# Performance work log

Measured on AMD Instinct MI355X. Metric: run time of the kernel, lower is better.

Reference implementation:

```python
import jax, jax.numpy as jnp
import numpy as np

BINS = 10


def _neg_pearson(p, t):
    # global standardization (torch.std default is unbiased, ddof=1)
    p = (p - p.mean()) / p.std(ddof=1)
    t = (t - t.mean()) / t.std(ddof=1)
    N = p.shape[1]
    sx = p.sum(1); sy = t.sum(1)
    sxy = (p * t).sum(1)
    sx2 = (p * p).sum(1); sy2 = (t * t).sum(1)
    pear = (N * sxy - sx * sy) / jnp.sqrt((N * sx2 - sx**2) * (N * sy2 - sy**2))
    return (1.0 - pear).mean()


def _hann(N):
    # torch.hann_window is periodic: 0.5*(1 - cos(2*pi*n/N))
    return 0.5 * (1.0 - jnp.cos(2.0 * jnp.pi * jnp.arange(N, dtype=jnp.float32) / N))


def _phase_correlation(x, t):
    # torch.stft with n_fft=seq_len, center=False, hann window -> single frame = rfft(x*hann)
    N = x.shape[1]
    w = _hann(N)
    xf = jnp.fft.rfft(x * w, axis=1)   # [B, N//2+1]
    tf = jnp.fft.rfft(t * w, axis=1)
    corr = xf * jnp.conj(tf)
    corr = corr / jnp.abs(corr)        # phase-only correlation
    cm = jnp.fft.irfft(corr, n=N, axis=1)  # [B, N]
    idx = jnp.argmax(cm, axis=1)
    return 1.0 - jnp.mean(jnp.cos(2.0 * jnp.pi * idx / N))


def _power_spectrum(x, t):
    xp = jnp.abs(jnp.fft.rfft(x, axis=1)) ** 2
    tp = jnp.abs(jnp.fft.rfft(t, axis=1)) ** 2
    return jnp.mean(jnp.abs(xp - tp)) / jnp.mean(tp)


def _mutual_information(x, y, bins=BINS):
    B, S = x.shape
    xmin = x.min(1); xmax = x.max(1)
    ymin = y.min(1); ymax = y.max(1)
    bwx = (xmax - xmin) / bins
    bwy = (ymax - ymin) / bins
    ix = jnp.clip(((x - xmin[:, None]) / bwx[:, None]).astype(jnp.int32), 0, bins - 1)
    iy = jnp.clip(((y - ymin[:, None]) / bwy[:, None]).astype(jnp.int32), 0, bins - 1)
    flat = ix * bins + iy  # [B, S]
    # vectorized 2D histogram via scatter-add (replaces the python double loop)
    hist = jax.vmap(lambda f: jnp.zeros(bins * bins, jnp.float32).at[f].add(1.0))(flat)
    hist = hist.reshape(B, bins, bins)
    hx = hist.sum(2); hy = hist.sum(1)
    denom = B * S  # NOTE: original normalizes by batch*seq (faithful reproduction)
    px = hx / denom; py = hy / denom; pxy = hist / denom
    eps = 1e-8
    mi = (pxy * jnp.log((pxy + eps) / (px[:, :, None] * py[:, None, :] + eps))).sum((1, 2))
    hxe = -(px * jnp.log(px + eps)).sum(1)
    hye = -(py * jnp.log(py + eps)).sum(1)
    nmi = mi / ((hxe + hye) / 2.0)
    return 1.0 - nmi.mean()


def setup_inputs() -> dict:
    key = jax.random.key(0)
    k1, k2 = jax.random.split(key)
    return {
        "predictions": jax.random.normal(k1, (2, 512, 16384), dtype=jnp.float32),
        "targets": jax.random.normal(k2, (512, 16384), dtype=jnp.float32),
        "i": 0,
        "epoch": 700,
    }


def reference(predictions, targets, i, epoch):
    p = predictions[i]  # [B, S]
    loss = _neg_pearson(p, targets)
    if epoch >= 400:
        loss = loss + _phase_correlation(p, targets)
        loss = loss + _power_spectrum(p, targets)
    if epoch >= 700:
        loss = loss + _mutual_information(p, targets)
    return loss
```

## Files before the change

kernel.cpp:

```cpp
#include <hip/hip_runtime.h>
#include <math.h>

#define BB 512
#define SS 16384
#define TPIF 6.28318530717958647692f

#define PD(i) ((i) + ((i) >> 4) + ((i) >> 8))
#define NPD 17472

__device__ __forceinline__ int digrev4(int n) {
    unsigned x = __brev((unsigned)n) >> (32 - 14);
    return (int)(((x & 0x1555u) << 1) | ((x >> 1) & 0x1555u));
}


template <int SGN, int LOG2Q>
__device__ __forceinline__ void stage_dif4(float2* sz, int t) {
    constexpr int Q = 1 << LOG2Q;
    const float sg = (float)SGN;
    #pragma unroll 2
    for (int c = 0; c < 4; ++c) {
        const int j = t + (c << 10);
        const int g = j >> LOG2Q;
        const int p = j & (Q - 1);
        const int e0 = (g << (LOG2Q + 2)) + p;
        const int i0 = PD(e0);
        const int i1 = PD(e0 + Q);
        const int i2 = PD(e0 + 2 * Q);
        const int i3 = PD(e0 + 3 * Q);
        float2 z0 = sz[i0], z1 = sz[i1], z2 = sz[i2], z3 = sz[i3];
        float t0r = z0.x + z2.x, t0i = z0.y + z2.y;
        float t1r = z0.x - z2.x, t1i = z0.y - z2.y;
        float t2r = z1.x + z3.x, t2i = z1.y + z3.y;
        float t3r = z1.x - z3.x, t3i = z1.y - z3.y;
        float b0r = t0r + t2r, b0i = t0i + t2i;
        float b2r = t0r - t2r, b2i = t0i - t2i;
        float b1r = t1r - sg * t3i, b1i = t1i + sg * t3r;
        float b3r = t1r + sg * t3i, b3i = t1i - sg * t3r;
        const float a = sg * (float)p * (1.0f / (4.0f * (float)Q));
        const float cb = __builtin_amdgcn_cosf(a);
        const float sb = __builtin_amdgcn_sinf(a);
        const float w2r = cb * cb - sb * sb, w2i = 2.0f * cb * sb;
        const float w3r = cb * w2r - sb * w2i, w3i = cb * w2i + sb * w2r;
        sz[i0] = make_float2(b0r, b0i);
        sz[i1] = make_float2(b1r * cb - b1i * sb,   b1r * sb + b1i * cb);
        sz[i2] = make_float2(b2r * w2r - b2i * w2i, b2r * w2i + b2i * w2r);
        sz[i3] = make_float2(b3r * w3r - b3i * w3i, b3r * w3i + b3i * w3r);
    }
    __syncthreads();
}

template <int SGN, int LOG2Q>
__device__ __forceinline__ void stage_dit4(float2* sz, int t) {
    constexpr int Q = 1 << LOG2Q;
    const float sg = (float)SGN;
    #pragma unroll 2
    for (int c = 0; c < 4; ++c) {
        const int j = t + (c << 10);
        const int g = j >> LOG2Q;
        const int p = j & (Q - 1);
        const int e0 = (g << (LOG2Q + 2)) + p;
        const int i0 = PD(e0);
        const int i1 = PD(e0 + Q);
        const int i2 = PD(e0 + 2 * Q);
        const int i3 = PD(e0 + 3 * Q);
        float2 z0 = sz[i0], z1 = sz[i1], z2 = sz[i2], z3 = sz[i3];
        const float a = sg * (float)p * (1.0f / (4.0f * (float)Q));
        const float cb = __builtin_amdgcn_cosf(a);
        const float sb = __builtin_amdgcn_sinf(a);
        const float w2r = cb * cb - sb * sb, w2i = 2.0f * cb * sb;
        const float w3r = cb * w2r - sb * w2i, w3i = cb * w2i + sb * w2r;
        float a1r = z1.x * cb - z1.y * sb,   a1i = z1.x * sb + z1.y * cb;
        float a2r = z2.x * w2r - z2.y * w2i, a2i = z2.x * w2i + z2.y * w2r;
        float a3r = z3.x * w3r - z3.y * w3i, a3i = z3.x * w3i + z3.y * w3r;
        float t0r = z0.x + a2r, t0i = z0.y + a2i;
        float t1r = z0.x - a2r, t1i = z0.y - a2i;
        float t2r = a1r + a3r, t2i = a1i + a3i;
        float t3r = a1r - a3r, t3i = a1i - a3i;
        sz[i0] = make_float2(t0r + t2r, t0i + t2i);
        sz[i2] = make_float2(t0r - t2r, t0i - t2i);
        sz[i1] = make_float2(t1r - sg * t3i, t1i + sg * t3r);
        sz[i3] = make_float2(t1r + sg * t3i, t1i - sg * t3r);
    }
    __syncthreads();
}

__global__ __launch_bounds__(1024, 4) void k_main(const float* __restrict__ pred,
                                                  const float* __restrict__ targ,
                                                  const int* __restrict__ ip,
                                                  float* __restrict__ wpear,
                                                  float* __restrict__ wcos,
                                                  double* __restrict__ wnum,
                                                  double* __restrict__ wden,
                                                  float* __restrict__ wnmi) {
    __shared__ float2 sz[NPD];
    __shared__ double dpart[16 * 5];
    __shared__ float fpart[16 * 4];
    __shared__ int   subhist[400];
    __shared__ float hxm[10], hym[10];
    __shared__ float mterm[128];
    __shared__ float sbounds[4];
    __shared__ float svalw[16];
    __shared__ int   sidxw[16];

    const int row = blockIdx.x;
    const int t = threadIdx.x;
    const int w = t >> 6;
    const int lane = t & 63;

    const float* xg = pred + (size_t)ip[0] * (size_t)BB * SS + (size_t)row * SS;
    const float* yg = targ + (size_t)row * SS;

    {
        const float4* xg4 = reinterpret_cast<const float4*>(xg);
        const float4* yg4 = reinterpret_cast<const float4*>(yg);
        double sx = 0, sy = 0, sxy = 0, sxx = 0, syy = 0;
        float xmn = 3.4e38f, xmx = -3.4e38f, ymn = 3.4e38f, ymx = -3.4e38f;
        #pragma unroll
        for (int m2 = 0; m2 < 4; ++m2) {
            int idx = t + (m2 << 10);
            float4 a = xg4[idx];
            float4 b = yg4[idx];
            int n0 = idx << 2;
            sz[PD(n0 + 0)] = make_float2(a.x, b.x);
            sz[PD(n0 + 1)] = make_float2(a.y, b.y);
            sz[PD(n0 + 2)] = make_float2(a.z, b.z);
            sz[PD(n0 + 3)] = make_float2(a.w, b.w);
            float av[4] = {a.x, a.y, a.z, a.w};
            float bv[4] = {b.x, b.y, b.z, b.w};
            #pragma unroll
            for (int c = 0; c < 4; ++c) {
                float aa = av[c], bb = bv[c];
                sx += (double)aa; sy += (double)bb;
                sxy += (double)aa * (double)bb;
                sxx += (double)aa * (double)aa;
                syy += (double)bb * (double)bb;
                xmn = fminf(xmn, aa); xmx = fmaxf(xmx, aa);
                ymn = fminf(ymn, bb); ymx = fmaxf(ymx, bb);
            }
        }
        #pragma unroll
        for (int o = 32; o > 0; o >>= 1) {
            sx += __shfl_down(sx, o, 64);  sy += __shfl_down(sy, o, 64);
            sxy += __shfl_down(sxy, o, 64);
            sxx += __shfl_down(sxx, o, 64); syy += __shfl_down(syy, o, 64);
            xmn = fminf(xmn, __shfl_down(xmn, o, 64));
            xmx = fmaxf(xmx, __shfl_down(xmx, o, 64));
            ymn = fminf(ymn, __shfl_down(ymn, o, 64));
            ymx = fmaxf(ymx, __shfl_down(ymx, o, 64));
        }
        if (lane == 0) {
            dpart[w*5+0] = sx; dpart[w*5+1] = sy; dpart[w*5+2] = sxy;
            dpart[w*5+3] = sxx; dpart[w*5+4] = syy;
            fpart[w*4+0] = xmn; fpart[w*4+1] = xmx; fpart[w*4+2] = ymn; fpart[w*4+3] = ymx;
        }
    }
    if (t < 400) subhist[t] = 0;
    __syncthreads();
    if (t == 0) {
        double v0=0,v1=0,v2=0,v3=0,v4=0;
        float b0=fpart[0], b1=fpart[1], b2=fpart[2], b3=fpart[3];
        for (int q = 0; q < 16; ++q) {
            v0 += dpart[q*5]; v1 += dpart[q*5+1]; v2 += dpart[q*5+2];
            v3 += dpart[q*5+3]; v4 += dpart[q*5+4];
            b0 = fminf(b0, fpart[q*4]);   b1 = fmaxf(b1, fpart[q*4+1]);
            b2 = fminf(b2, fpart[q*4+2]); b3 = fmaxf(b3, fpart[q*4+3]);
        }
        double N = (double)SS;
        double num = N * v2 - v0 * v1;
        double den = sqrt((N * v3 - v0 * v0) * (N * v4 - v1 * v1));
        wpear[row] = (float)(1.0 - num / den);
        sbounds[0] = b0; sbounds[1] = b1; sbounds[2] = b2; sbounds[3] = b3;
    }
    __syncthreads();

    {
        const float x0 = sbounds[0], bwx = (sbounds[1] - x0) / 10.0f;
        const float y0 = sbounds[2], bwy = (sbounds[3] - y0) / 10.0f;
        int* hsub = subhist + ((t >> 6) & 3) * 100;
        #pragma unroll 2
        for (int m = 0; m < 16; ++m) {
            float2 v = sz[PD(t + (m << 10))];
            int ix = (int)((v.x - x0) / bwx); ix = min(max(ix, 0), 9);
            int iy = (int)((v.y - y0) / bwy); iy = min(max(iy, 0), 9);
            atomicAdd(&hsub[ix * 10 + iy], 1);
        }
    }
    __syncthreads();
    if (t < 100) subhist[t] = subhist[t] + subhist[100+t] + subhist[200+t] + subhist[300+t];
    __syncthreads();
    if (t < 10) {
        int s1 = 0, s2 = 0;
        for (int j = 0; j < 10; ++j) { s1 += subhist[t*10+j]; s2 += subhist[j*10+t]; }
        hxm[t] = (float)s1; hym[t] = (float)s2;
    }
    __syncthreads();
    {
        float term = 0.0f;
        if (t < 100) {
            const float denom = 8388608.0f, eps = 1e-8f;
            float pxy = (float)subhist[t] / denom;
            float px = hxm[t / 10] / denom, py = hym[t % 10] / denom;
            term = pxy * logf((pxy + eps) / (px * py + eps));
        }
        if (t < 128) mterm[t] = (t < 100) ? term : 0.0f;
    }
    __syncthreads();
    if (t == 0) {
        const float denom = 8388608.0f, eps = 1e-8f;
        float mi = 0.0f;
        for (int q = 0; q < 100; ++q) mi += mterm[q];
        float hxe = 0.0f, hye = 0.0f;
        for (int q = 0; q < 10; ++q) {
            float px = hxm[q] / denom, py = hym[q] / denom;
            hxe -= px * logf(px + eps);
            hye -= py * logf(py + eps);
        }
        wnmi[row] = mi / (0.5f * (hxe + hye));
    }
    __syncthreads();

    stage_dif4<-1, 12>(sz, t);
    stage_dif4<-1, 10>(sz, t);
    stage_dif4<-1,  8>(sz, t);
    stage_dif4<-1,  6>(sz, t);
    stage_dif4<-1,  4>(sz, t);
    stage_dif4<-1,  2>(sz, t);
    stage_dif4<-1,  0>(sz, t);

    {
        double anum = 0.0, aden = 0.0;
        float crv[8], civ[8];
        #pragma unroll 1
        for (int m = 0; m < 8; ++m) {
            int k = t + (m << 10);
            int km = (SS - k) & (SS - 1);
            int qa = digrev4(k), qb = digrev4(km);
            float2 za = sz[PD(qa)];
            float2 zb = sz[PD(qb)];
            float ar  = za.x, ai  = za.y;
            float cr0 = zb.x, ci0 = zb.y;
            float xr = 0.5f * (ar + cr0), xi = 0.5f * (ai - ci0);
            float yr = 0.5f * (ai + ci0), yi = 0.5f * (cr0 - ar);
            float xp = xr * xr + xi * xi;
            float tp = yr * yr + yi * yi;
            anum += (double)fabsf(xp - tp);
            aden += (double)tp;
            float2 zap = sz[PD(digrev4((k + 1) & (SS - 1)))];
            float2 zam = sz[PD(digrev4((k - 1) & (SS - 1)))];
            float2 zbp = sz[PD(digrev4((km + 1) & (SS - 1)))];
            float2 zbm = sz[PD(digrev4((km - 1) & (SS - 1)))];
            float zwr = 0.5f * ar  - 0.25f * (zap.x + zam.x);
            float zwi = 0.5f * ai  - 0.25f * (zap.y + zam.y);
            float vwr = 0.5f * cr0 - 0.25f * (zbp.x + zbm.x);
            float vwi = 0.5f * ci0 - 0.25f * (zbp.y + zbm.y);
            float xwr = 0.5f * (zwr + vwr), xwi = 0.5f * (zwi - vwi);
            float ywr = 0.5f * (zwi + vwi), ywi = 0.5f * (vwr - zwr);
            float cr = xwr * ywr + xwi * ywi;
            float ci = xwi * ywr - xwr * ywi;
            float mag = sqrtf(cr * cr + ci * ci);
            crv[m] = cr / mag; civ[m] = ci / mag;
        }
        float c8 = 0.0f;
        if (t == 0) {
            float2 z0 = sz[PD(digrev4(8192))];
            float2 zp = sz[PD(digrev4(8193))];
            float2 zm = sz[PD(digrev4(8191))];
            float ar = z0.x, ai = z0.y;
            anum += (double)fabsf(ar * ar - ai * ai);
            aden += (double)(ai * ai);
            float zwr = 0.5f * ar - 0.25f * (zp.x + zm.x);
            float zwi = 0.5f * ai - 0.25f * (zp.y + zm.y);
            float pr = zwr * zwi;
            c8 = pr / fabsf(pr);
        }
        #pragma unroll
        for (int o = 32; o > 0; o >>= 1) {
            anum += __shfl_down(anum, o, 64);
            aden += __shfl_down(aden, o, 64);
        }
        if (lane == 0) { dpart[w*2] = anum; dpart[w*2+1] = aden; }
        __syncthreads();
        #pragma unroll
        for (int m = 0; m < 8; ++m) {
            int k = t + (m << 10);
            int km = (SS - k) & (SS - 1);
            int q = digrev4(k), q2 = digrev4(km);
            sz[PD(q)]  = make_float2(crv[m],  civ[m]);
            sz[PD(q2)] = make_float2(crv[m], -civ[m]);
        }
        if (t == 0) {
            sz[PD(digrev4(8192))] = make_float2(c8, 0.0f);
            double a = 0, b = 0;
            for (int q2_ = 0; q2_ < 16; ++q2_) { a += dpart[q2_*2]; b += dpart[q2_*2+1]; }
            wnum[row] = a; wden[row] = b;
        }
    }
    __syncthreads();

    stage_dit4<1,  0>(sz, t);
    stage_dit4<1,  2>(sz, t);
    stage_dit4<1,  4>(sz, t);
    stage_dit4<1,  6>(sz, t);
    stage_dit4<1,  8>(sz, t);
    stage_dit4<1, 10>(sz, t);
    stage_dit4<1, 12>(sz, t);

    {
        float bv = -3.4e38f; int bi = 0;
        #pragma unroll
        for (int m = 0; m < 16; ++m) {
            int n = t + (m << 10);
            float v = sz[PD(n)].x;
            if (v > bv) { bv = v; bi = n; }
        }
        #pragma unroll
        for (int o = 32; o > 0; o >>= 1) {
            float v2 = __shfl_down(bv, o, 64);
            int i2 = __shfl_down(bi, o, 64);
            if (v2 > bv || (v2 == bv && i2 < bi)) { bv = v2; bi = i2; }
        }
        if (lane == 0) { svalw[w] = bv; sidxw[w] = bi; }
    }
    __syncthreads();
    if (t == 0) {
        float bv = svalw[0]; int bi = sidxw[0];
        for (int q = 1; q < 16; ++q) {
            if (svalw[q] > bv || (svalw[q] == bv && sidxw[q] < bi)) { bv = svalw[q]; bi = sidxw[q]; }
        }
        wcos[row] = cosf(TPIF * (float)bi / 16384.0f);
    }
}

__global__ __launch_bounds__(512) void k_combine(const float* __restrict__ wpear,
                                                 const float* __restrict__ wcos,
                                                 const double* __restrict__ wnum,
                                                 const double* __restrict__ wden,
                                                 const float* __restrict__ wnmi,
                                                 const int* __restrict__ ep,
                                                 float* __restrict__ out) {
    __shared__ double dp[8 * 5];
    const int tid = threadIdx.x;
    const int w = tid >> 6, lane = tid & 63;
    double v0 = (double)wpear[tid], v1 = (double)wcos[tid];
    double v2 = wnum[tid], v3 = wden[tid], v4 = (double)wnmi[tid];
    #pragma unroll
    for (int o = 32; o > 0; o >>= 1) {
        v0 += __shfl_down(v0, o, 64); v1 += __shfl_down(v1, o, 64);
        v2 += __shfl_down(v2, o, 64); v3 += __shfl_down(v3, o, 64);
        v4 += __shfl_down(v4, o, 64);
    }
    if (lane == 0) {
        dp[w*5+0] = v0; dp[w*5+1] = v1; dp[w*5+2] = v2; dp[w*5+3] = v3; dp[w*5+4] = v4;
    }
    __syncthreads();
    if (tid == 0) {
        double s0=0,s1=0,s2=0,s3=0,s4=0;
        for (int q = 0; q < 8; ++q) {
            s0 += dp[q*5]; s1 += dp[q*5+1]; s2 += dp[q*5+2]; s3 += dp[q*5+3]; s4 += dp[q*5+4];
        }
        int epoch = ep[0];
        double loss = s0 / 512.0;
        if (epoch >= 400) {
            loss += 1.0 - s1 / 512.0;
            loss += s2 / s3;
        }
        if (epoch >= 700) {
            loss += 1.0 - s4 / 512.0;
        }
        out[0] = (float)loss;
    }
}

extern "C" void kernel_launch(void* const* d_in, const int* in_sizes, int n_in,
                              void* d_out, int out_size, void* d_ws, size_t ws_size,
                              hipStream_t stream) {
    const float* pred = (const float*)d_in[0];
    const float* targ = (const float*)d_in[1];
    const int* ip = (const int*)d_in[2];
    const int* ep = (const int*)d_in[3];
    float* out = (float*)d_out;

    double* wnum = (double*)d_ws;
    double* wden = wnum + BB;
    float* wpear = (float*)(wden + BB);
    float* wcos = wpear + BB;
    float* wnmi = wcos + BB;

    k_main<<<dim3(BB), dim3(1024), 0, stream>>>(pred, targ, ip, wpear, wcos, wnum, wden, wnmi);
    k_combine<<<dim3(1), dim3(512), 0, stream>>>(wpear, wcos, wnum, wden, wnmi, ep, out);
}
```

Before: 208.3 us.

## Switch shared-memory FFT from radix-4 to radix-8 stages

Replaces the seven radix-4 DIF/DIT stages of the 16384-point in-LDS FFT with four radix-8 stages plus one twiddle-free radix-4 stage, and updates the digit-reversed index mapping to match. Fewer stages mean fewer LDS passes and fewer __syncthreads barriers. Each radix-8 butterfly also computes one sincos and derives the other twiddles by recurrence. The cost is higher register pressure per thread, under launch_bounds(1024,4), and possible bank conflicts from the new strides.

```diff
diff --git a/kernel.cpp b/kernel.cpp
--- a/kernel.cpp
+++ b/kernel.cpp
@@ -8,79 +8,171 @@
 #define PD(i) ((i) + ((i) >> 4) + ((i) >> 8))
 #define NPD 17472
 
-__device__ __forceinline__ int digrev4(int n) {
-    unsigned x = __brev((unsigned)n) >> (32 - 14);
-    return (int)(((x & 0x1555u) << 1) | ((x >> 1) & 0x1555u));
+__device__ __forceinline__ int sp(int k) {
+    int s = ((k & 7) << 11) + (((k >> 3) & 7) << 8) + (((k >> 6) & 7) << 5)
+          + (((k >> 9) & 7) << 2) + ((k >> 12) & 3);
+    return PD(s);
 }
 
 
 template <int SGN, int LOG2Q>
-__device__ __forceinline__ void stage_dif4(float2* sz, int t) {
+__device__ __forceinline__ void stage_dif8(float2* sz, int t) {
     constexpr int Q = 1 << LOG2Q;
+    constexpr int DQ = Q + (Q >> 4) + (Q >> 8);
     const float sg = (float)SGN;
-    #pragma unroll 2
-    for (int c = 0; c < 4; ++c) {
+    const float r2 = 0.70710678118654752f;
+    #pragma unroll 1
+    for (int c = 0; c < 2; ++c) {
         const int j = t + (c << 10);
         const int g = j >> LOG2Q;
         const int p = j & (Q - 1);
-        const int e0 = (g << (LOG2Q + 2)) + p;
-        const int i0 = PD(e0);
-        const int i1 = PD(e0 + Q);
-        const int i2 = PD(e0 + 2 * Q);
-        const int i3 = PD(e0 + 3 * Q);
-        float2 z0 = sz[i0], z1 = sz[i1], z2 = sz[i2], z3 = sz[i3];
+        const int i0 = PD((g << (LOG2Q + 3)) + p);
+        int idx[8];
+        #pragma unroll
+        for (int k = 0; k < 8; ++k)
+            idx[k] = (LOG2Q >= 4) ? (i0 + k * DQ) : (i0 + 4 * k + (k >> 2));
+        float2 z[8];
+        #pragma unroll
+        for (int k = 0; k < 8; ++k) z[k] = sz[idx[k]];
+        float2 a0, a1, a2, a3, b0, b1, b2, b3;
+        a0 = make_float2(z[0].x + z[4].x, z[0].y + z[4].y);
+        b0 = make_float2(z[0].x - z[4].x, z[0].y - z[4].y);
+        a1 = make_float2(z[1].x + z[5].x, z[1].y + z[5].y);
+        b1 = make_float2(z[1].x - z[5].x, z[1].y - z[5].y);
+        a2 = make_float2(z[2].x + z[6].x, z[2].y + z[6].y);
+        b2 = make_float2(z[2].x - z[6].x, z[2].y - z[6].y);
+        a3 = make_float2(z[3].x + z[7].x, z[3].y + z[7].y);
+        b3 = make_float2(z[3].x - z[7].x, z[3].y - z[7].y);
+        { float x = b1.x, y = b1.y; b1 = make_float2(r2 * (x - sg * y), r2 * (y + sg * x)); }
+        { float x = b2.x, y = b2.y; b2 = make_float2(-sg * y, sg * x); }
+        { float x = b3.x, y = b3.y; b3 = make_float2(-r2 * (x + sg * y), r2 * (sg * x - y)); }
+        float2 o[8];
+        {
+            float t0r = a0.x + a2.x, t0i = a0.y + a2.y;
+            float t1r = a0.x - a2.x, t1i = a0.y - a2.y;
+            float t2r = a1.x + a3.x, t2i = a1.y + a3.y;
+            float t3r = a1.x - a3.x, t3i = a1.y - a3.y;
+            o[0] = make_float2(t0r + t2r, t0i + t2i);
+            o[4] = make_float2(t0r - t2r, t0i - t2i);
+            o[2] = make_float2(t1r - sg * t3i, t1i + sg * t3r);
+            o[6] = make_float2(t1r + sg * t3i, t1i - sg * t3r);
+        }
+        {
+            float t0r = b0.x + b2.x, t0i = b0.y + b2.y;
+            float t1r = b0.x - b2.x, t1i = b0.y - b2.y;
+            float t2r = b1.x + b3.x, t2i = b1.y + b3.y;
+            float t3r = b1.x - b3.x, t3i = b1.y - b3.y;
+            o[1] = make_float2(t0r + t2r, t0i + t2i);
+            o[5] = make_float2(t0r - t2r, t0i - t2i);
+            o[3] = make_float2(t1r - sg * t3i, t1i + sg * t3r);
+            o[7] = make_float2(t1r + sg * t3i, t1i - sg * t3r);
+        }
+        const float arev = sg * (float)p * (1.0f / (8.0f * (float)Q));
+        const float cb = __builtin_amdgcn_cosf(arev);
+        const float sb = __builtin_amdgcn_sinf(arev);
+        sz[idx[0]] = o[0];
+        float wr = cb, wi = sb;
+        #pragma unroll
+        for (int r = 1; r < 8; ++r) {
+            sz[idx[r]] = make_float2(o[r].x * wr - o[r].y * wi,
+                                     o[r].x * wi + o[r].y * wr);
+            float nr = wr * cb - wi * sb, ni = wr * sb + wi * cb;
+            wr = nr; wi = ni;
+        }
+    }
+    __syncthreads();
+}
+
+template <int SGN, int LOG2Q>
+__device__ __forceinline__ void stage_dit8(float2* sz, int t) {
+    constexpr int Q = 1 << LOG2Q;
+    constexpr int DQ = Q + (Q >> 4) + (Q >> 8);
+    const float sg = (float)SGN;
+    const float r2 = 0.70710678118654752f;
+    #pragma unroll 1
+    for (int c = 0; c < 2; ++c) {
+        const int j = t + (c << 10);
+        const int g = j >> LOG2Q;
+        const int p = j & (Q - 1);
+        const int i0 = PD((g << (LOG2Q + 3)) + p);
+        int idx[8];
+        #pragma unroll
+        for (int k = 0; k < 8; ++k)
+            idx[k] = (LOG2Q >= 4) ? (i0 + k * DQ) : (i0 + 4 * k + (k >> 2));
+        const float arev = sg * (float)p * (1.0f / (8.0f * (float)Q));
+        const float cb = __builtin_amdgcn_cosf(arev);
+        const float sb = __builtin_amdgcn_sinf(arev);
+        float2 z[8];
+        z[0] = sz[idx[0]];
+        float wr = cb, wi = sb;
+        #pragma unroll
+        for (int k = 1; k < 8; ++k) {
+            float2 v = sz[idx[k]];
+            z[k] = make_float2(v.x * wr - v.y * wi, v.x * wi + v.y * wr);
+            float nr = wr * cb - wi * sb, ni = wr * sb + wi * cb;
+            wr = nr; wi = ni;
+        }
+        float2 U0, U1, U2, U3, V0, V1, V2, V3;
+        {
+            float t0r = z[0].x + z[4].x, t0i = z[0].y + z[4].y;
+            float t1r = z[0].x - z[4].x, t1i = z[0].y - z[4].y;
+            float t2r = z[2].x + z[6].x, t2i = z[2].y + z[6].y;
+            float t3r = z[2].x - z[6].x, t3i = z[2].y - z[6].y;
+            U0 = make_float2(t0r + t2r, t0i + t2i);
+            U2 = make_float2(t0r - t2r, t0i - t2i);
+            U1 = make_float2(t1r - sg * t3i, t1i + sg * t3r);
+            U3 = make_float2(t1r + sg * t3i, t1i - sg * t3r);
+        }
+        {
+            float t0r = z[1].x + z[5].x, t0i = z[1].y + z[5].y;
+            float t1r = z[1].x - z[5].x, t1i = z[1].y - z[5].y;
+            float t2r = z[3].x + z[7].x, t2i = z[3].y + z[7].y;
+            float t3r = z[3].x - z[7].x, t3i = z[3].y - z[7].y;
+            V0 = make_float2(t0r + t2r, t0i + t2i);
+            V2 = make_float2(t0r - t2r, t0i - t2i);
+            V1 = make_float2(t1r - sg * t3i, t1i + sg * t3r);
+            V3 = make_float2(t1r + sg * t3i, t1i - sg * t3r);
+        }
+        {
+            float2 tw = V0;
+            sz[idx[0]] = make_float2(U0.x + tw.x, U0.y + tw.y);
+            sz[idx[4]] = make_float2(U0.x - tw.x, U0.y - tw.y);
+        }
+        {
+            float2 tw = make_float2(r2 * (V1.x - sg * V1.y), r2 * (V1.y + sg * V1.x));
+            sz[idx[1]] = make_float2(U1.x + tw.x, U1.y + tw.y);
+            sz[idx[5]] = make_float2(U1.x - tw.x, U1.y - tw.y);
+        }
+        {
+            float2 tw = make_float2(-sg * V2.y, sg * V2.x);
+            sz[idx[2]] = make_float2(U2.x + tw.x, U2.y + tw.y);
+            sz[idx[6]] = make_float2(U2.x - tw.x, U2.y - tw.y);
+        }
+        {
+            float2 tw = make_float2(-r2 * (V3.x + sg * V3.y), r2 * (sg * V3.x - V3.y));
+            sz[idx[3]] = make_float2(U3.x + tw.x, U3.y + tw.y);
+            sz[idx[7]] = make_float2(U3.x - tw.x, U3.y - tw.y);
+        }
+    }
+    __syncthreads();
+}
+
+template <int SGN>
+__device__ __forceinline__ void stage_nt4(float2* sz, int t) {
+    const float sg = (float)SGN;
+    #pragma unroll 1
+    for (int c = 0; c < 4; ++c) {
+        const int j = t + (c << 10);
+        const int i0 = 4 * j + (j >> 2) + (j >> 6);
+        float2 z0 = sz[i0], z1 = sz[i0 + 1], z2 = sz[i0 + 2], z3 = sz[i0 + 3];
         float t0r = z0.x + z2.x, t0i = z0.y + z2.y;
         float t1r = z0.x - z2.x, t1i = z0.y - z2.y;
         float t2r = z1.x + z3.x, t2i = z1.y + z3.y;
         float t3r = z1.x - z3.x, t3i = z1.y - z3.y;
-        float b0r = t0r + t2r, b0i = t0i + t2i;
-        float b2r = t0r - t2r, b2i = t0i - t2i;
-        float b1r = t1r - sg * t3i, b1i = t1i + sg * t3r;
-        float b3r = t1r + sg * t3i, b3i = t1i - sg * t3r;
-        const float a = sg * (float)p * (1.0f / (4.0f * (float)Q));
-        const float cb = __builtin_amdgcn_cosf(a);
-        const float sb = __builtin_amdgcn_sinf(a);
-        const float w2r = cb * cb - sb * sb, w2i = 2.0f * cb * sb;
-        const float w3r = cb * w2r - sb * w2i, w3i = cb * w2i + sb * w2r;
-        sz[i0] = make_float2(b0r, b0i);
-        sz[i1] = make_float2(b1r * cb - b1i * sb,   b1r * sb + b1i * cb);
-        sz[i2] = make_float2(b2r * w2r - b2i * w2i, b2r * w2i + b2i * w2r);
-        sz[i3] = make_float2(b3r * w3r - b3i * w3i, b3r * w3i + b3i * w3r);
-    }
-    __syncthreads();
-}
-
-template <int SGN, int LOG2Q>
-__device__ __forceinline__ void stage_dit4(float2* sz, int t) {
-    constexpr int Q = 1 << LOG2Q;
-    const float sg = (float)SGN;
-    #pragma unroll 2
-    for (int c = 0; c < 4; ++c) {
-        const int j = t + (c << 10);
-        const int g = j >> LOG2Q;
-        const int p = j & (Q - 1);
-        const int e0 = (g << (LOG2Q + 2)) + p;
-        const int i0 = PD(e0);
-        const int i1 = PD(e0 + Q);
-        const int i2 = PD(e0 + 2 * Q);
-        const int i3 = PD(e0 + 3 * Q);
-        float2 z0 = sz[i0], z1 = sz[i1], z2 = sz[i2], z3 = sz[i3];
-        const float a = sg * (float)p * (1.0f / (4.0f * (float)Q));
-        const float cb = __builtin_amdgcn_cosf(a);
-        const float sb = __builtin_amdgcn_sinf(a);
-        const float w2r = cb * cb - sb * sb, w2i = 2.0f * cb * sb;
-        const float w3r = cb * w2r - sb * w2i, w3i = cb * w2i + sb * w2r;
-        float a1r = z1.x * cb - z1.y * sb,   a1i = z1.x * sb + z1.y * cb;
-        float a2r = z2.x * w2r - z2.y * w2i, a2i = z2.x * w2i + z2.y * w2r;
-        float a3r = z3.x * w3r - z3.y * w3i, a3i = z3.x * w3i + z3.y * w3r;
-        float t0r = z0.x + a2r, t0i = z0.y + a2i;
-        float t1r = z0.x - a2r, t1i = z0.y - a2i;
-        float t2r = a1r + a3r, t2i = a1i + a3i;
-        float t3r = a1r - a3r, t3i = a1i - a3i;
-        sz[i0] = make_float2(t0r + t2r, t0i + t2i);
-        sz[i2] = make_float2(t0r - t2r, t0i - t2i);
-        sz[i1] = make_float2(t1r - sg * t3i, t1i + sg * t3r);
-        sz[i3] = make_float2(t1r + sg * t3i, t1i - sg * t3r);
+        sz[i0]     = make_float2(t0r + t2r, t0i + t2i);
+        sz[i0 + 2] = make_float2(t0r - t2r, t0i - t2i);
+        sz[i0 + 1] = make_float2(t1r - sg * t3i, t1i + sg * t3r);
+        sz[i0 + 3] = make_float2(t1r + sg * t3i, t1i - sg * t3r);
     }
     __syncthreads();
 }
@@ -220,13 +312,11 @@
     }
     __syncthreads();
 
-    stage_dif4<-1, 12>(sz, t);
-    stage_dif4<-1, 10>(sz, t);
-    stage_dif4<-1,  8>(sz, t);
-    stage_dif4<-1,  6>(sz, t);
-    stage_dif4<-1,  4>(sz, t);
-    stage_dif4<-1,  2>(sz, t);
-    stage_dif4<-1,  0>(sz, t);
+    stage_dif8<-1, 11>(sz, t);
+    stage_dif8<-1,  8>(sz, t);
+    stage_dif8<-1,  5>(sz, t);
+    stage_dif8<-1,  2>(sz, t);
+    stage_nt4<-1>(sz, t);
 
     {
         double anum = 0.0, aden = 0.0;
@@ -235,9 +325,8 @@
         for (int m = 0; m < 8; ++m) {
             int k = t + (m << 10);
             int km = (SS - k) & (SS - 1);
-            int qa = digrev4(k), qb = digrev4(km);
-            float2 za = sz[PD(qa)];
-            float2 zb = sz[PD(qb)];
+            float2 za = sz[sp(k)];
+            float2 zb = sz[sp(km)];
             float ar  = za.x, ai  = za.y;
             float cr0 = zb.x, ci0 = zb.y;
             float xr = 0.5f * (ar + cr0), xi = 0.5f * (ai - ci0);
@@ -246,10 +335,10 @@
             float tp = yr * yr + yi * yi;
             anum += (double)fabsf(xp - tp);
             aden += (double)tp;
-            float2 zap = sz[PD(digrev4((k + 1) & (SS - 1)))];
-            float2 zam = sz[PD(digrev4((k - 1) & (SS - 1)))];
-            float2 zbp = sz[PD(digrev4((km + 1) & (SS - 1)))];
-            float2 zbm = sz[PD(digrev4((km - 1) & (SS - 1)))];
+            float2 zap = sz[sp((k + 1) & (SS - 1))];
+            float2 zam = sz[sp((k - 1) & (SS - 1))];
+            float2 zbp = sz[sp((km + 1) & (SS - 1))];
+            float2 zbm = sz[sp((km - 1) & (SS - 1))];
             float zwr = 0.5f * ar  - 0.25f * (zap.x + zam.x);
             float zwi = 0.5f * ai  - 0.25f * (zap.y + zam.y);
             float vwr = 0.5f * cr0 - 0.25f * (zbp.x + zbm.x);
@@ -263,9 +352,9 @@
         }
         float c8 = 0.0f;
         if (t == 0) {
-            float2 z0 = sz[PD(digrev4(8192))];
-            float2 zp = sz[PD(digrev4(8193))];
-            float2 zm = sz[PD(digrev4(8191))];
+            float2 z0 = sz[sp(8192)];
+            float2 zp = sz[sp(8193)];
+            float2 zm = sz[sp(8191)];
             float ar = z0.x, ai = z0.y;
             anum += (double)fabsf(ar * ar - ai * ai);
             aden += (double)(ai * ai);
@@ -285,12 +374,11 @@
         for (int m = 0; m < 8; ++m) {
             int k = t + (m << 10);
             int km = (SS - k) & (SS - 1);
-            int q = digrev4(k), q2 = digrev4(km);
-            sz[PD(q)]  = make_float2(crv[m],  civ[m]);
-            sz[PD(q2)] = make_float2(crv[m], -civ[m]);
+            sz[sp(k)]  = make_float2(crv[m],  civ[m]);
+            sz[sp(km)] = make_float2(crv[m], -civ[m]);
         }
         if (t == 0) {
-            sz[PD(digrev4(8192))] = make_float2(c8, 0.0f);
+            sz[sp(8192)] = make_float2(c8, 0.0f);
             double a = 0, b = 0;
             for (int q2_ = 0; q2_ < 16; ++q2_) { a += dpart[q2_*2]; b += dpart[q2_*2+1]; }
             wnum[row] = a; wden[row] = b;
@@ -298,13 +386,11 @@
     }
     __syncthreads();
 
-    stage_dit4<1,  0>(sz, t);
-    stage_dit4<1,  2>(sz, t);
-    stage_dit4<1,  4>(sz, t);
-    stage_dit4<1,  6>(sz, t);
-    stage_dit4<1,  8>(sz, t);
-    stage_dit4<1, 10>(sz, t);
-    stage_dit4<1, 12>(sz, t);
+    stage_nt4<1>(sz, t);
+    stage_dit8<1,  2>(sz, t);
+    stage_dit8<1,  5>(sz, t);
+    stage_dit8<1,  8>(sz, t);
+    stage_dit8<1, 11>(sz, t);
 
     {
         float bv = -3.4e38f; int bi = 0;
```

After: 199.3 us. 4.3% less time.
